# Optimization experiments

Measured on AMD Instinct MI355X. Metric: run time of the kernel, lower is better.

Reference implementation:

```python
import jax, jax.numpy as jnp
import numpy as np

N_NODES = 50000
IN_CH = 128
OUT_CH = 64
HEADS = 2
N_EDGES = 400000
NEG_SLOPE = 0.2  # PyG GATConv default


def _glorot(key, shape):
    fan_in, fan_out = shape[0], shape[-1]
    lim = jnp.sqrt(6.0 / (fan_in + fan_out))
    return jax.random.uniform(key, shape, jnp.float32, -lim, lim)


def setup_inputs() -> dict:
    key = jax.random.key(0)
    ks = jax.random.split(key, 12)
    hid = 2 * OUT_CH  # per-head channels of conv1
    inp = {
        "x": jax.random.normal(ks[0], (N_NODES, IN_CH), jnp.float32),
        "edge_index": jax.random.randint(ks[1], (2, N_EDGES), 0, N_NODES, jnp.int32),
        # conv1: in=IN_CH, out=hid per head, HEADS heads, concat
        "W1": _glorot(ks[2], (IN_CH, HEADS * hid)),
        "att_src1": _glorot(ks[3], (HEADS, hid)),
        "att_dst1": _glorot(ks[4], (HEADS, hid)),
        "b1": jnp.zeros((HEADS * hid,), jnp.float32),
        # conv_mu: in=hid*HEADS, out=OUT_CH, 1 head
        "W_mu": _glorot(ks[5], (hid * HEADS, OUT_CH)),
        "att_src_mu": _glorot(ks[6], (1, OUT_CH)),
        "att_dst_mu": _glorot(ks[7], (1, OUT_CH)),
        "b_mu": jnp.zeros((OUT_CH,), jnp.float32),
        # conv_logstd: same shapes as conv_mu
        "W_ls": _glorot(ks[8], (hid * HEADS, OUT_CH)),
        "att_src_ls": _glorot(ks[9], (1, OUT_CH)),
        "att_dst_ls": _glorot(ks[10], (1, OUT_CH)),
        "b_ls": jnp.zeros((OUT_CH,), jnp.float32),
    }
    return inp


def gat_conv(x, src, dst, W, att_src, att_dst, b, n_nodes):
    """PyG GATConv (add_self_loops handled by caller in src/dst)."""
    H, C = att_src.shape
    h = (x @ W).reshape(n_nodes, H, C)                       # [N,H,C]
    a_src = jnp.einsum('nhc,hc->nh', h, att_src)             # [N,H]
    a_dst = jnp.einsum('nhc,hc->nh', h, att_dst)
    e = jax.nn.leaky_relu(a_src[src] + a_dst[dst], NEG_SLOPE)  # [E,H]
    # scatter-softmax over incoming edges per destination node
    m = jax.ops.segment_max(e, dst, num_segments=n_nodes)
    e = jnp.exp(e - m[dst])
    denom = jax.ops.segment_sum(e, dst, num_segments=n_nodes)
    alpha = e / (denom[dst] + 1e-16)                          # [E,H]
    out = jax.ops.segment_sum(h[src] * alpha[:, :, None], dst,
                              num_segments=n_nodes)           # [N,H,C]
    return out.reshape(n_nodes, H * C) + b


def reference(x, edge_index, W1, att_src1, att_dst1, b1,
              W_mu, att_src_mu, att_dst_mu, b_mu,
              W_ls, att_src_ls, att_dst_ls, b_ls):
    n = x.shape[0]
    loop = jnp.arange(n, dtype=edge_index.dtype)
    src = jnp.concatenate([edge_index[0], loop])  # add self-loops (PyG default)
    dst = jnp.concatenate([edge_index[1], loop])
    h = jax.nn.elu(gat_conv(x, src, dst, W1, att_src1, att_dst1, b1, n))
    mu = gat_conv(h, src, dst, W_mu, att_src_mu, att_dst_mu, b_mu, n)
    logstd = gat_conv(h, src, dst, W_ls, att_src_ls, att_dst_ls, b_ls, n)
    return (mu, logstd)
```

## Files before the change

kernel.cpp:

```cpp
#include <hip/hip_runtime.h>
#include <math.h>

#define N_NODES 50000
#define N_EDGES 400000
#define PAD 64

typedef __attribute__((ext_vector_type(8))) short bf16x8;
typedef __attribute__((ext_vector_type(4))) float f32x4;

__device__ __forceinline__ float lrelu(float x){ return x > 0.f ? x : 0.2f*x; }
__device__ __forceinline__ float bf2f(unsigned short u){ return __uint_as_float(((unsigned int)u)<<16); }
__device__ __forceinline__ unsigned short f2bf(float f){
    unsigned int b = __float_as_uint(f);
    return (unsigned short)((b + 0x7FFFu + ((b>>16)&1u)) >> 16);
}
__device__ __forceinline__ float4 bf4(ushort4 u){
    return make_float4(bf2f(u.x), bf2f(u.y), bf2f(u.z), bf2f(u.w));
}
__device__ __forceinline__ float wexp(float e){ return __expf(fminf(e, 80.f)); }

__global__ __launch_bounds__(256) void init_k(const float* __restrict__ W1,
        const float* __restrict__ Wmu, const float* __restrict__ Wls,
        const float* __restrict__ attS, const float* __restrict__ attD,
        unsigned short* __restrict__ W1T, unsigned short* __restrict__ WmlT,
        float* __restrict__ V1, int* __restrict__ counts){
    int i = blockIdx.x*256 + threadIdx.x;
    if (i < N_NODES) counts[i] = 0;
    if (i < 32768){
        int nn = i >> 7, k = i & 127;
        W1T[i] = f2bf(W1[k*256 + nn]);
        int n2 = i >> 8, k2 = i & 255;
        float v = (n2 < 64) ? Wmu[k2*64 + n2] : Wls[k2*64 + (n2-64)];
        WmlT[i] = f2bf(v);
    }
    if (blockIdx.x == 0){
        for (int idx = threadIdx.x; idx < 512; idx += 256){
            int v = idx >> 7, k = idx & 127;
            int h = v & 1;
            const float* attp = (v >> 1) ? attD : attS;
            float s = 0.f;
            #pragma unroll 8
            for (int c = 0; c < 128; c++)
                s = fmaf(W1[k*256 + h*128 + c], attp[h*128 + c], s);
            V1[idx] = s;
        }
    }
}

__global__ __launch_bounds__(256) void prep_k(const float* __restrict__ x, unsigned short* __restrict__ xb,
        const float* __restrict__ V1, float2* __restrict__ as1, float2* __restrict__ ad1,
        const int* __restrict__ src, const int* __restrict__ dst,
        int* __restrict__ counts, int* __restrict__ csr_src){
    int t = threadIdx.x;
    int gthr = blockIdx.x*256 + t;
    int n = blockIdx.x*8 + (t >> 5);
    int lane = t & 31;

    float4 xv = ((const float4*)(x + (size_t)n*128))[lane];
    ((ushort4*)(xb + (size_t)n*128))[lane] = make_ushort4(f2bf(xv.x), f2bf(xv.y), f2bf(xv.z), f2bf(xv.w));
    int c0 = lane*4;
    float s0 = xv.x*V1[      c0] + xv.y*V1[      c0+1] + xv.z*V1[      c0+2] + xv.w*V1[      c0+3];
    float s1 = xv.x*V1[128 + c0] + xv.y*V1[128 + c0+1] + xv.z*V1[128 + c0+2] + xv.w*V1[128 + c0+3];
    float d0 = xv.x*V1[256 + c0] + xv.y*V1[256 + c0+1] + xv.z*V1[256 + c0+2] + xv.w*V1[256 + c0+3];
    float d1 = xv.x*V1[384 + c0] + xv.y*V1[384 + c0+1] + xv.z*V1[384 + c0+2] + xv.w*V1[384 + c0+3];
    #pragma unroll
    for (int m = 1; m < 32; m <<= 1){
        s0 += __shfl_xor(s0, m, 32);
        s1 += __shfl_xor(s1, m, 32);
        d0 += __shfl_xor(d0, m, 32);
        d1 += __shfl_xor(d1, m, 32);
    }
    if (lane == 0){
        as1[n] = make_float2(s0, s1);
        ad1[n] = make_float2(d0, d1);
    }

    if (gthr < N_EDGES){
        int d = dst[gthr];
        int pos = atomicAdd(&counts[d], 1);
        csr_src[d*PAD + pos] = src[gthr];
    }
}

__global__ __launch_bounds__(256) void agg1x_k(const unsigned short* __restrict__ xb,
        const float2* __restrict__ as, const float2* __restrict__ ad,
        const int* __restrict__ counts, const int* __restrict__ csr_src,
        unsigned short* __restrict__ aggx0, unsigned short* __restrict__ aggx1){
    int wave = threadIdx.x >> 6, lane = threadIdx.x & 63;
    int n = blockIdx.x*4 + wave;
    if (n >= N_NODES) return;

    float2 adn = ad[n], asn = as[n];
    float w0s = wexp(lrelu(asn.x + adn.x));
    float w1s = wexp(lrelu(asn.y + adn.y));
    float l0 = w0s, l1 = w1s;

    ushort2 u = ((const ushort2*)(xb + (size_t)n*128))[lane];
    float rx = bf2f(u.x), ry = bf2f(u.y);
    float a0x = w0s*rx, a0y = w0s*ry;
    float a1x = w1s*rx, a1y = w1s*ry;

    int deg = counts[n];
    int off = n*PAD;
    int dm1 = deg - 1;
    for (int k = 0; k < deg; k += 4){
        int s0 = csr_src[off + k];
        int s1 = csr_src[off + min(k+1, dm1)];
        int s2 = csr_src[off + min(k+2, dm1)];
        int s3 = csr_src[off + min(k+3, dm1)];
        float2 e0 = as[s0], e1 = as[s1], e2 = as[s2], e3 = as[s3];
        ushort2 u0 = ((const ushort2*)(xb + (size_t)s0*128))[lane];
        ushort2 u1 = ((const ushort2*)(xb + (size_t)s1*128))[lane];
        ushort2 u2 = ((const ushort2*)(xb + (size_t)s2*128))[lane];
        ushort2 u3 = ((const ushort2*)(xb + (size_t)s3*128))[lane];
        float w00 = wexp(lrelu(e0.x + adn.x));
        float w01 = wexp(lrelu(e0.y + adn.y));
        float w10 = (k+1 <= dm1) ? wexp(lrelu(e1.x + adn.x)) : 0.f;
        float w11 = (k+1 <= dm1) ? wexp(lrelu(e1.y + adn.y)) : 0.f;
        float w20 = (k+2 <= dm1) ? wexp(lrelu(e2.x + adn.x)) : 0.f;
        float w21 = (k+2 <= dm1) ? wexp(lrelu(e2.y + adn.y)) : 0.f;
        float w30 = (k+3 <= dm1) ? wexp(lrelu(e3.x + adn.x)) : 0.f;
        float w31 = (k+3 <= dm1) ? wexp(lrelu(e3.y + adn.y)) : 0.f;
        l0 += (w00 + w10) + (w20 + w30);
        l1 += (w01 + w11) + (w21 + w31);
        float r0x = bf2f(u0.x), r0y = bf2f(u0.y);
        float r1x = bf2f(u1.x), r1y = bf2f(u1.y);
        float r2x = bf2f(u2.x), r2y = bf2f(u2.y);
        float r3x = bf2f(u3.x), r3y = bf2f(u3.y);
        a0x = fmaf(w00, r0x, a0x); a0y = fmaf(w00, r0y, a0y);
        a1x = fmaf(w01, r0x, a1x); a1y = fmaf(w01, r0y, a1y);
        a0x = fmaf(w10, r1x, a0x); a0y = fmaf(w10, r1y, a0y);
        a1x = fmaf(w11, r1x, a1x); a1y = fmaf(w11, r1y, a1y);
        a0x = fmaf(w20, r2x, a0x); a0y = fmaf(w20, r2y, a0y);
        a1x = fmaf(w21, r2x, a1x); a1y = fmaf(w21, r2y, a1y);
        a0x = fmaf(w30, r3x, a0x); a0y = fmaf(w30, r3y, a0y);
        a1x = fmaf(w31, r3x, a1x); a1y = fmaf(w31, r3y, a1y);
    }

    float i0 = 1.f / (l0 + 1e-16f);
    float i1 = 1.f / (l1 + 1e-16f);
    ((ushort2*)(aggx0 + (size_t)n*128))[lane] = make_ushort2(f2bf(a0x*i0), f2bf(a0y*i0));
    ((ushort2*)(aggx1 + (size_t)n*128))[lane] = make_ushort2(f2bf(a1x*i1), f2bf(a1y*i1));
}

template<int MODE>
__global__ __launch_bounds__(256) void mfma_gemm_k(const unsigned short* __restrict__ A0,
        const unsigned short* __restrict__ A1,
        const unsigned short* __restrict__ BT, unsigned short* __restrict__ C,
        int M, int K, int ldc, const float* __restrict__ bias,
        const float* __restrict__ attS0, const float* __restrict__ attD0,
        const float* __restrict__ attS1, const float* __restrict__ attD1,
        float* __restrict__ outS, float* __restrict__ outD){
    __shared__ unsigned short As[128*40];
    __shared__ unsigned short Bs[128*40];
    int t = threadIdx.x;
    int lane = t & 63, wid = t >> 6;
    int wy = wid >> 1, wx = wid & 1;
    int quad = lane >> 4, l15 = lane & 15;
    int row0 = blockIdx.y * 128;
    int col0 = blockIdx.x * 128;
    const unsigned short* A = (MODE == 0 && blockIdx.x) ? A1 : A0;

    f32x4 acc[4][4];
    #pragma unroll
    for (int i = 0; i < 4; i++)
        #pragma unroll
        for (int j = 0; j < 4; j++)
            acc[i][j] = (f32x4){0.f, 0.f, 0.f, 0.f};

    int r = t >> 2;
    int cofs = (t & 3) * 8;

    for (int k0 = 0; k0 < K; k0 += 32){
        int gr0 = min(row0 + r,      M-1);
        int gr1 = min(row0 + r + 64, M-1);
        float4 av0 = *(const float4*)(A  + (size_t)gr0*K + k0 + cofs);
        float4 av1 = *(const float4*)(A  + (size_t)gr1*K + k0 + cofs);
        float4 bv0 = *(const float4*)(BT + (size_t)(col0 + r)*K      + k0 + cofs);
        float4 bv1 = *(const float4*)(BT + (size_t)(col0 + r + 64)*K + k0 + cofs);
        __syncthreads();
        *(float4*)&As[r*40 + cofs]      = av0;
        *(float4*)&As[(r+64)*40 + cofs] = av1;
        *(float4*)&Bs[r*40 + cofs]      = bv0;
        *(float4*)&Bs[(r+64)*40 + cofs] = bv1;
        __syncthreads();

        bf16x8 af[4], bf[4];
        #pragma unroll
        for (int i = 0; i < 4; i++)
            af[i] = *(const bf16x8*)&As[(wy*64 + i*16 + l15)*40 + quad*8];
        #pragma unroll
        for (int j = 0; j < 4; j++)
            bf[j] = *(const bf16x8*)&Bs[(wx*64 + j*16 + l15)*40 + quad*8];
        #pragma unroll
        for (int i = 0; i < 4; i++)
            #pragma unroll
            for (int j = 0; j < 4; j++)
                acc[i][j] = __builtin_amdgcn_mfma_f32_16x16x32_bf16(af[i], bf[j], acc[i][j], 0, 0, 0);
    }

    float aS[4], aD[4], bvals[4];
    #pragma unroll
    for (int j = 0; j < 4; j++){
        int cc = col0 + wx*64 + j*16 + l15;
        if (MODE == 0){
            bvals[j] = bias[cc];
        } else {
            int c2 = j*16 + l15;
            aS[j] = wx ? attS1[c2] : attS0[c2];
            aD[j] = wx ? attD1[c2] : attD0[c2];
        }
    }

    #pragma unroll
    for (int i = 0; i < 4; i++){
        #pragma unroll
        for (int reg = 0; reg < 4; reg++){
            int rr = row0 + wy*64 + i*16 + quad*4 + reg;
            if (MODE == 0){
                if (rr < M){
                    #pragma unroll
                    for (int j = 0; j < 4; j++){
                        int cc = col0 + wx*64 + j*16 + l15;
                        float v = acc[i][j][reg] + bvals[j];
                        v = v > 0.f ? v : __expf(v) - 1.f;
                        C[(size_t)rr*ldc + cc] = f2bf(v);
                    }
                }
            } else {
                float sp = 0.f, dp = 0.f;
                #pragma unroll
                for (int j = 0; j < 4; j++){
                    float v = acc[i][j][reg];
                    int cc = col0 + wx*64 + j*16 + l15;
                    if (rr < M) C[(size_t)rr*ldc + cc] = f2bf(v);
                    sp = fmaf(v, aS[j], sp);
                    dp = fmaf(v, aD[j], dp);
                }
                #pragma unroll
                for (int msk = 1; msk < 16; msk <<= 1){
                    sp += __shfl_xor(sp, msk);
                    dp += __shfl_xor(dp, msk);
                }
                if (l15 == 0 && rr < M){
                    outS[rr*2 + wx] = sp;
                    outD[rr*2 + wx] = dp;
                }
            }
        }
    }
}

__global__ __launch_bounds__(256) void agg2_k(const unsigned short* __restrict__ hml,
        const float* __restrict__ as, const float* __restrict__ ad,
        const int* __restrict__ counts, const int* __restrict__ csr_src,
        const float* __restrict__ b_mu, const float* __restrict__ b_ls,
        float* __restrict__ out){
    int grp = threadIdx.x >> 5, lane = threadIdx.x & 31;
    int n = blockIdx.x*8 + grp;
    if (n >= N_NODES) return;
    int g = lane >> 4;
    const ushort4* hv = (const ushort4*)hml;

    float adh = ad[n*2 + g];
    float ash = as[n*2 + g];

    float w = wexp(lrelu(ash + adh));
    float l = w;
    float4 r = bf4(hv[(size_t)n*32 + lane]);
    float4 acc = make_float4(w*r.x, w*r.y, w*r.z, w*r.w);

    int deg = counts[n];
    int off = n*PAD;
    int dm1 = deg - 1;
    for (int k = 0; k < deg; k += 4){
        int s0 = csr_src[off + k];
        int s1 = csr_src[off + min(k+1, dm1)];
        int s2 = csr_src[off + min(k+2, dm1)];
        int s3 = csr_src[off + min(k+3, dm1)];
        float e0 = as[s0*2 + g], e1 = as[s1*2 + g];
        float e2 = as[s2*2 + g], e3 = as[s3*2 + g];
        float4 r0 = bf4(hv[(size_t)s0*32 + lane]);
        float4 r1 = bf4(hv[(size_t)s1*32 + lane]);
        float4 r2 = bf4(hv[(size_t)s2*32 + lane]);
        float4 r3 = bf4(hv[(size_t)s3*32 + lane]);
        float w0 = wexp(lrelu(e0 + adh));
        float w1 = (k+1 <= dm1) ? wexp(lrelu(e1 + adh)) : 0.f;
        float w2 = (k+2 <= dm1) ? wexp(lrelu(e2 + adh)) : 0.f;
        float w3 = (k+3 <= dm1) ? wexp(lrelu(e3 + adh)) : 0.f;
        l += (w0 + w1) + (w2 + w3);
        acc.x = fmaf(w0, r0.x, acc.x); acc.x = fmaf(w1, r1.x, acc.x);
        acc.x = fmaf(w2, r2.x, acc.x); acc.x = fmaf(w3, r3.x, acc.x);
        acc.y = fmaf(w0, r0.y, acc.y); acc.y = fmaf(w1, r1.y, acc.y);
        acc.y = fmaf(w2, r2.y, acc.y); acc.y = fmaf(w3, r3.y, acc.y);
        acc.z = fmaf(w0, r0.z, acc.z); acc.z = fmaf(w1, r1.z, acc.z);
        acc.z = fmaf(w2, r2.z, acc.z); acc.z = fmaf(w3, r3.z, acc.z);
        acc.w = fmaf(w0, r0.w, acc.w); acc.w = fmaf(w1, r1.w, acc.w);
        acc.w = fmaf(w2, r2.w, acc.w); acc.w = fmaf(w3, r3.w, acc.w);
    }

    float invl = 1.f / (l + 1e-16f);
    int c = (lane & 15) * 4;
    const float* bb = g ? b_ls : b_mu;
    float4 b4 = *(const float4*)&bb[c];
    float4 v;
    v.x = acc.x*invl + b4.x; v.y = acc.y*invl + b4.y;
    v.z = acc.z*invl + b4.z; v.w = acc.w*invl + b4.w;
    float* base = g ? (out + (size_t)N_NODES*64) : out;
    *(float4*)&base[(size_t)n*64 + c] = v;
}

extern "C" void kernel_launch(void* const* d_in, const int* in_sizes, int n_in,
                              void* d_out, int out_size, void* d_ws, size_t ws_size,
                              hipStream_t stream) {
    const float* x           = (const float*)d_in[0];
    const int*   ei          = (const int*)d_in[1];
    const float* W1          = (const float*)d_in[2];
    const float* att_src1    = (const float*)d_in[3];
    const float* att_dst1    = (const float*)d_in[4];
    const float* b1          = (const float*)d_in[5];
    const float* W_mu        = (const float*)d_in[6];
    const float* att_src_mu  = (const float*)d_in[7];
    const float* att_dst_mu  = (const float*)d_in[8];
    const float* b_mu        = (const float*)d_in[9];
    const float* W_ls        = (const float*)d_in[10];
    const float* att_src_ls  = (const float*)d_in[11];
    const float* att_dst_ls  = (const float*)d_in[12];
    const float* b_ls        = (const float*)d_in[13];
    float* out = (float*)d_out;

    const int* srcp = ei;
    const int* dstp = ei + N_EDGES;

    unsigned short* xb    = (unsigned short*)d_ws;
    unsigned short* aggx0 = xb    + (size_t)N_NODES*128;
    unsigned short* aggx1 = aggx0 + (size_t)N_NODES*128;
    unsigned short* hbuf  = aggx1 + (size_t)N_NODES*128;
    unsigned short* hml   = hbuf  + (size_t)N_NODES*256;
    unsigned short* W1T   = hml   + (size_t)N_NODES*128;
    unsigned short* WmlT  = W1T   + 32768;
    int*   counts = (int*)(WmlT + 32768);
    float2* as1   = (float2*)(counts + N_NODES);
    float2* ad1   = as1 + N_NODES;
    float*  as2   = (float*)(ad1 + N_NODES);
    float*  ad2   = as2 + 2*N_NODES;
    float*  V1    = ad2 + 2*N_NODES;
    int*    csr   = (int*)(V1 + 512);

    init_k<<<196, 256, 0, stream>>>(W1, W_mu, W_ls, att_src1, att_dst1, W1T, WmlT, V1, counts);

    prep_k<<<6250, 256, 0, stream>>>(x, xb, V1, as1, ad1, srcp, dstp, counts, csr);

    agg1x_k<<<(N_NODES + 3) / 4, 256, 0, stream>>>(xb, as1, ad1, counts, csr, aggx0, aggx1);

    mfma_gemm_k<0><<<dim3(2, 391), 256, 0, stream>>>(aggx0, aggx1, W1T, hbuf, N_NODES, 128, 256,
                                                     b1, nullptr, nullptr, nullptr, nullptr,
                                                     nullptr, nullptr);

    mfma_gemm_k<2><<<dim3(1, 391), 256, 0, stream>>>(hbuf, hbuf, WmlT, hml, N_NODES, 256, 128,
                                                     nullptr, att_src_mu, att_dst_mu,
                                                     att_src_ls, att_dst_ls, as2, ad2);

    agg2_k<<<(N_NODES + 7) / 8, 256, 0, stream>>>(hml, as2, ad2, counts, csr, b_mu, b_ls, out);
}
```

Measured before the change: 228.1 us.

## Fuse init, prep and layer-1 aggregation into one cooperative persistent kernel

Merges the three front kernels (weight transpose/V1 init, x conversion plus CSR build, layer-1 attention aggregation) into a single cooperative kernel that uses grid.sync between phases and grid-stride loops. This removes two kernel launches and their inter-kernel gaps. In exchange the grid is capped by occupancy (occ*256 blocks), so the gather-heavy aggregation runs as a persistent loop, and the cooperative launch with grid-wide barriers adds overhead. The grid size assumes 256 CUs.

```diff
diff --git a/kernel.cpp b/kernel.cpp
--- a/kernel.cpp
+++ b/kernel.cpp
@@ -1,5 +1,8 @@
 #include <hip/hip_runtime.h>
+#include <hip/hip_cooperative_groups.h>
 #include <math.h>
+
+namespace cg = cooperative_groups;
 
 #define N_NODES 50000
 #define N_EDGES 400000
@@ -19,128 +22,125 @@
 }
 __device__ __forceinline__ float wexp(float e){ return __expf(fminf(e, 80.f)); }
 
-__global__ __launch_bounds__(256) void init_k(const float* __restrict__ W1,
-        const float* __restrict__ Wmu, const float* __restrict__ Wls,
+__global__ __launch_bounds__(256) void front_k(
+        const float* __restrict__ x, const int* __restrict__ src, const int* __restrict__ dst,
+        const float* __restrict__ W1, const float* __restrict__ Wmu, const float* __restrict__ Wls,
         const float* __restrict__ attS, const float* __restrict__ attD,
+        unsigned short* __restrict__ xb,
         unsigned short* __restrict__ W1T, unsigned short* __restrict__ WmlT,
-        float* __restrict__ V1, int* __restrict__ counts){
-    int i = blockIdx.x*256 + threadIdx.x;
-    if (i < N_NODES) counts[i] = 0;
-    if (i < 32768){
+        float* __restrict__ V1, int* __restrict__ counts, int* __restrict__ csr_src,
+        float2* __restrict__ as1, float2* __restrict__ ad1,
+        unsigned short* __restrict__ aggx0, unsigned short* __restrict__ aggx1)
+{
+    cg::grid_group grid = cg::this_grid();
+    const int tid = threadIdx.x, bid = blockIdx.x, nb = gridDim.x;
+    const int gthr = bid*256 + tid, gsz = nb*256;
+
+    for (int i = gthr; i < N_NODES; i += gsz) counts[i] = 0;
+    for (int i = gthr; i < 32768; i += gsz){
         int nn = i >> 7, k = i & 127;
         W1T[i] = f2bf(W1[k*256 + nn]);
         int n2 = i >> 8, k2 = i & 255;
         float v = (n2 < 64) ? Wmu[k2*64 + n2] : Wls[k2*64 + (n2-64)];
         WmlT[i] = f2bf(v);
     }
-    if (blockIdx.x == 0){
-        for (int idx = threadIdx.x; idx < 512; idx += 256){
-            int v = idx >> 7, k = idx & 127;
-            int h = v & 1;
-            const float* attp = (v >> 1) ? attD : attS;
-            float s = 0.f;
-            #pragma unroll 8
-            for (int c = 0; c < 128; c++)
-                s = fmaf(W1[k*256 + h*128 + c], attp[h*128 + c], s);
-            V1[idx] = s;
-        }
-    }
-}
-
-__global__ __launch_bounds__(256) void prep_k(const float* __restrict__ x, unsigned short* __restrict__ xb,
-        const float* __restrict__ V1, float2* __restrict__ as1, float2* __restrict__ ad1,
-        const int* __restrict__ src, const int* __restrict__ dst,
-        int* __restrict__ counts, int* __restrict__ csr_src){
-    int t = threadIdx.x;
-    int gthr = blockIdx.x*256 + t;
-    int n = blockIdx.x*8 + (t >> 5);
-    int lane = t & 31;
-
-    float4 xv = ((const float4*)(x + (size_t)n*128))[lane];
-    ((ushort4*)(xb + (size_t)n*128))[lane] = make_ushort4(f2bf(xv.x), f2bf(xv.y), f2bf(xv.z), f2bf(xv.w));
-    int c0 = lane*4;
-    float s0 = xv.x*V1[      c0] + xv.y*V1[      c0+1] + xv.z*V1[      c0+2] + xv.w*V1[      c0+3];
-    float s1 = xv.x*V1[128 + c0] + xv.y*V1[128 + c0+1] + xv.z*V1[128 + c0+2] + xv.w*V1[128 + c0+3];
-    float d0 = xv.x*V1[256 + c0] + xv.y*V1[256 + c0+1] + xv.z*V1[256 + c0+2] + xv.w*V1[256 + c0+3];
-    float d1 = xv.x*V1[384 + c0] + xv.y*V1[384 + c0+1] + xv.z*V1[384 + c0+2] + xv.w*V1[384 + c0+3];
-    #pragma unroll
-    for (int m = 1; m < 32; m <<= 1){
-        s0 += __shfl_xor(s0, m, 32);
-        s1 += __shfl_xor(s1, m, 32);
-        d0 += __shfl_xor(d0, m, 32);
-        d1 += __shfl_xor(d1, m, 32);
-    }
-    if (lane == 0){
-        as1[n] = make_float2(s0, s1);
-        ad1[n] = make_float2(d0, d1);
-    }
-
-    if (gthr < N_EDGES){
-        int d = dst[gthr];
+    if (gthr < 512){
+        int v = gthr >> 7, k = gthr & 127;
+        int h = v & 1;
+        const float* attp = (v >> 1) ? attD : attS;
+        float s = 0.f;
+        #pragma unroll 8
+        for (int c = 0; c < 128; c++)
+            s = fmaf(W1[k*256 + h*128 + c], attp[h*128 + c], s);
+        V1[gthr] = s;
+    }
+    grid.sync();
+
+    for (int g = bid; g < 6250; g += nb){
+        int n = g*8 + (tid >> 5);
+        int lane = tid & 31;
+        float4 xv = ((const float4*)(x + (size_t)n*128))[lane];
+        ((ushort4*)(xb + (size_t)n*128))[lane] = make_ushort4(f2bf(xv.x), f2bf(xv.y), f2bf(xv.z), f2bf(xv.w));
+        int c0 = lane*4;
+        float s0 = xv.x*V1[      c0] + xv.y*V1[      c0+1] + xv.z*V1[      c0+2] + xv.w*V1[      c0+3];
+        float s1 = xv.x*V1[128 + c0] + xv.y*V1[128 + c0+1] + xv.z*V1[128 + c0+2] + xv.w*V1[128 + c0+3];
+        float d0 = xv.x*V1[256 + c0] + xv.y*V1[256 + c0+1] + xv.z*V1[256 + c0+2] + xv.w*V1[256 + c0+3];
+        float d1 = xv.x*V1[384 + c0] + xv.y*V1[384 + c0+1] + xv.z*V1[384 + c0+2] + xv.w*V1[384 + c0+3];
+        #pragma unroll
+        for (int m = 1; m < 32; m <<= 1){
+            s0 += __shfl_xor(s0, m, 32);
+            s1 += __shfl_xor(s1, m, 32);
+            d0 += __shfl_xor(d0, m, 32);
+            d1 += __shfl_xor(d1, m, 32);
+        }
+        if (lane == 0){
+            as1[n] = make_float2(s0, s1);
+            ad1[n] = make_float2(d0, d1);
+        }
+    }
+    for (int e = gthr; e < N_EDGES; e += gsz){
+        int d = dst[e];
         int pos = atomicAdd(&counts[d], 1);
-        csr_src[d*PAD + pos] = src[gthr];
-    }
-}
-
-__global__ __launch_bounds__(256) void agg1x_k(const unsigned short* __restrict__ xb,
-        const float2* __restrict__ as, const float2* __restrict__ ad,
-        const int* __restrict__ counts, const int* __restrict__ csr_src,
-        unsigned short* __restrict__ aggx0, unsigned short* __restrict__ aggx1){
-    int wave = threadIdx.x >> 6, lane = threadIdx.x & 63;
-    int n = blockIdx.x*4 + wave;
-    if (n >= N_NODES) return;
-
-    float2 adn = ad[n], asn = as[n];
-    float w0s = wexp(lrelu(asn.x + adn.x));
-    float w1s = wexp(lrelu(asn.y + adn.y));
-    float l0 = w0s, l1 = w1s;
-
-    ushort2 u = ((const ushort2*)(xb + (size_t)n*128))[lane];
-    float rx = bf2f(u.x), ry = bf2f(u.y);
-    float a0x = w0s*rx, a0y = w0s*ry;
-    float a1x = w1s*rx, a1y = w1s*ry;
-
-    int deg = counts[n];
-    int off = n*PAD;
-    int dm1 = deg - 1;
-    for (int k = 0; k < deg; k += 4){
-        int s0 = csr_src[off + k];
-        int s1 = csr_src[off + min(k+1, dm1)];
-        int s2 = csr_src[off + min(k+2, dm1)];
-        int s3 = csr_src[off + min(k+3, dm1)];
-        float2 e0 = as[s0], e1 = as[s1], e2 = as[s2], e3 = as[s3];
-        ushort2 u0 = ((const ushort2*)(xb + (size_t)s0*128))[lane];
-        ushort2 u1 = ((const ushort2*)(xb + (size_t)s1*128))[lane];
-        ushort2 u2 = ((const ushort2*)(xb + (size_t)s2*128))[lane];
-        ushort2 u3 = ((const ushort2*)(xb + (size_t)s3*128))[lane];
-        float w00 = wexp(lrelu(e0.x + adn.x));
-        float w01 = wexp(lrelu(e0.y + adn.y));
-        float w10 = (k+1 <= dm1) ? wexp(lrelu(e1.x + adn.x)) : 0.f;
-        float w11 = (k+1 <= dm1) ? wexp(lrelu(e1.y + adn.y)) : 0.f;
-        float w20 = (k+2 <= dm1) ? wexp(lrelu(e2.x + adn.x)) : 0.f;
-        float w21 = (k+2 <= dm1) ? wexp(lrelu(e2.y + adn.y)) : 0.f;
-        float w30 = (k+3 <= dm1) ? wexp(lrelu(e3.x + adn.x)) : 0.f;
-        float w31 = (k+3 <= dm1) ? wexp(lrelu(e3.y + adn.y)) : 0.f;
-        l0 += (w00 + w10) + (w20 + w30);
-        l1 += (w01 + w11) + (w21 + w31);
-        float r0x = bf2f(u0.x), r0y = bf2f(u0.y);
-        float r1x = bf2f(u1.x), r1y = bf2f(u1.y);
-        float r2x = bf2f(u2.x), r2y = bf2f(u2.y);
-        float r3x = bf2f(u3.x), r3y = bf2f(u3.y);
-        a0x = fmaf(w00, r0x, a0x); a0y = fmaf(w00, r0y, a0y);
-        a1x = fmaf(w01, r0x, a1x); a1y = fmaf(w01, r0y, a1y);
-        a0x = fmaf(w10, r1x, a0x); a0y = fmaf(w10, r1y, a0y);
-        a1x = fmaf(w11, r1x, a1x); a1y = fmaf(w11, r1y, a1y);
-        a0x = fmaf(w20, r2x, a0x); a0y = fmaf(w20, r2y, a0y);
-        a1x = fmaf(w21, r2x, a1x); a1y = fmaf(w21, r2y, a1y);
-        a0x = fmaf(w30, r3x, a0x); a0y = fmaf(w30, r3y, a0y);
-        a1x = fmaf(w31, r3x, a1x); a1y = fmaf(w31, r3y, a1y);
-    }
-
-    float i0 = 1.f / (l0 + 1e-16f);
-    float i1 = 1.f / (l1 + 1e-16f);
-    ((ushort2*)(aggx0 + (size_t)n*128))[lane] = make_ushort2(f2bf(a0x*i0), f2bf(a0y*i0));
-    ((ushort2*)(aggx1 + (size_t)n*128))[lane] = make_ushort2(f2bf(a1x*i1), f2bf(a1y*i1));
+        csr_src[d*PAD + pos] = src[e];
+    }
+    grid.sync();
+
+    for (int g = bid; g < 12500; g += nb){
+        int n = g*4 + (tid >> 6);
+        int lane = tid & 63;
+
+        float2 adn = ad1[n], asn = as1[n];
+        float w0s = wexp(lrelu(asn.x + adn.x));
+        float w1s = wexp(lrelu(asn.y + adn.y));
+        float l0 = w0s, l1 = w1s;
+
+        ushort2 u = ((const ushort2*)(xb + (size_t)n*128))[lane];
+        float rx = bf2f(u.x), ry = bf2f(u.y);
+        float a0x = w0s*rx, a0y = w0s*ry;
+        float a1x = w1s*rx, a1y = w1s*ry;
+
+        int deg = counts[n];
+        int off = n*PAD;
+        int dm1 = deg - 1;
+        for (int k = 0; k < deg; k += 4){
+            int s0 = csr_src[off + k];
+            int s1 = csr_src[off + min(k+1, dm1)];
+            int s2 = csr_src[off + min(k+2, dm1)];
+            int s3 = csr_src[off + min(k+3, dm1)];
+            float2 e0 = as1[s0], e1 = as1[s1], e2 = as1[s2], e3 = as1[s3];
+            ushort2 u0 = ((const ushort2*)(xb + (size_t)s0*128))[lane];
+            ushort2 u1 = ((const ushort2*)(xb + (size_t)s1*128))[lane];
+            ushort2 u2 = ((const ushort2*)(xb + (size_t)s2*128))[lane];
+            ushort2 u3 = ((const ushort2*)(xb + (size_t)s3*128))[lane];
+            float w00 = wexp(lrelu(e0.x + adn.x));
+            float w01 = wexp(lrelu(e0.y + adn.y));
+            float w10 = (k+1 <= dm1) ? wexp(lrelu(e1.x + adn.x)) : 0.f;
+            float w11 = (k+1 <= dm1) ? wexp(lrelu(e1.y + adn.y)) : 0.f;
+            float w20 = (k+2 <= dm1) ? wexp(lrelu(e2.x + adn.x)) : 0.f;
+            float w21 = (k+2 <= dm1) ? wexp(lrelu(e2.y + adn.y)) : 0.f;
+            float w30 = (k+3 <= dm1) ? wexp(lrelu(e3.x + adn.x)) : 0.f;
+            float w31 = (k+3 <= dm1) ? wexp(lrelu(e3.y + adn.y)) : 0.f;
+            l0 += (w00 + w10) + (w20 + w30);
+            l1 += (w01 + w11) + (w21 + w31);
+            float r0x = bf2f(u0.x), r0y = bf2f(u0.y);
+            float r1x = bf2f(u1.x), r1y = bf2f(u1.y);
+            float r2x = bf2f(u2.x), r2y = bf2f(u2.y);
+            float r3x = bf2f(u3.x), r3y = bf2f(u3.y);
+            a0x = fmaf(w00, r0x, a0x); a0y = fmaf(w00, r0y, a0y);
+            a1x = fmaf(w01, r0x, a1x); a1y = fmaf(w01, r0y, a1y);
+            a0x = fmaf(w10, r1x, a0x); a0y = fmaf(w10, r1y, a0y);
+            a1x = fmaf(w11, r1x, a1x); a1y = fmaf(w11, r1y, a1y);
+            a0x = fmaf(w20, r2x, a0x); a0y = fmaf(w20, r2y, a0y);
+            a1x = fmaf(w21, r2x, a1x); a1y = fmaf(w21, r2y, a1y);
+            a0x = fmaf(w30, r3x, a0x); a0y = fmaf(w30, r3y, a0y);
+            a1x = fmaf(w31, r3x, a1x); a1y = fmaf(w31, r3y, a1y);
+        }
+
+        float i0 = 1.f / (l0 + 1e-16f);
+        float i1 = 1.f / (l1 + 1e-16f);
+        ((ushort2*)(aggx0 + (size_t)n*128))[lane] = make_ushort2(f2bf(a0x*i0), f2bf(a0y*i0));
+        ((ushort2*)(aggx1 + (size_t)n*128))[lane] = make_ushort2(f2bf(a1x*i1), f2bf(a1y*i1));
+    }
 }
 
 template<int MODE>
@@ -347,11 +347,22 @@
     float*  V1    = ad2 + 2*N_NODES;
     int*    csr   = (int*)(V1 + 512);
 
-    init_k<<<196, 256, 0, stream>>>(W1, W_mu, W_ls, att_src1, att_dst1, W1T, WmlT, V1, counts);
-
-    prep_k<<<6250, 256, 0, stream>>>(x, xb, V1, as1, ad1, srcp, dstp, counts, csr);
-
-    agg1x_k<<<(N_NODES + 3) / 4, 256, 0, stream>>>(xb, as1, ad1, counts, csr, aggx0, aggx1);
+    int occ = 0;
+    if (hipOccupancyMaxActiveBlocksPerMultiprocessor(&occ, (const void*)front_k, 256, 0) != hipSuccess || occ < 1)
+        occ = 1;
+    int grid = occ * 256;
+    if (grid > 12500) grid = 12500;
+
+    void* args[] = {
+        (void*)&x, (void*)&srcp, (void*)&dstp,
+        (void*)&W1, (void*)&W_mu, (void*)&W_ls,
+        (void*)&att_src1, (void*)&att_dst1,
+        (void*)&xb, (void*)&W1T, (void*)&WmlT,
+        (void*)&V1, (void*)&counts, (void*)&csr,
+        (void*)&as1, (void*)&ad1,
+        (void*)&aggx0, (void*)&aggx1
+    };
+    hipLaunchCooperativeKernel((const void*)front_k, dim3(grid), dim3(256), args, 0, stream);
 
     mfma_gemm_k<0><<<dim3(2, 391), 256, 0, stream>>>(aggx0, aggx1, W1T, hbuf, N_NODES, 128, 256,
                                                      b1, nullptr, nullptr, nullptr, nullptr,
```

After: 447.9 us. 96.4% more time.
